# Kernel tuning notes

Measured on AMD Instinct MI355X. Metric: run time of the kernel, lower is better.

Reference implementation:

```python
import jax, jax.numpy as jnp
import numpy as np

H = 256  # GRU hidden size


def _gru_scan(state, lengths, Wih, Whh, bih, bhh):
    # state: [B, T, D]; run a batched GRU over time, freezing h once t >= lengths[b]
    B, T, D = state.shape
    # precompute input gates for all timesteps: [T, B, 3H]
    gi_all = jnp.einsum('btd,gd->tbg', state, Wih) + bih

    def step(h, inp):
        gi, t = inp
        gh = h @ Whh.T + bhh                       # [B, 3H]
        i_r, i_z, i_n = jnp.split(gi, 3, axis=-1)
        h_r, h_z, h_n = jnp.split(gh, 3, axis=-1)
        r = jax.nn.sigmoid(i_r + h_r)
        z = jax.nn.sigmoid(i_z + h_z)
        n = jnp.tanh(i_n + r * h_n)
        h_new = (1.0 - z) * n + z * h              # torch GRUCell update
        mask = (t < lengths)[:, None]              # ragged: stop updating past length
        return jnp.where(mask, h_new, h), None

    h0 = jnp.zeros((B, H), state.dtype)
    h, _ = jax.lax.scan(step, h0, (gi_all, jnp.arange(T)))
    return h  # [B, H] = hidden after lengths[b] GRU steps


def _mlp(x, w1, b1, w2, b2, w3, b3, w4, b4, wq, bq):
    x = jax.nn.relu(x @ w1.T + b1)
    x = jax.nn.relu(x @ w2.T + b2)
    x = jax.nn.relu(x @ w3.T + b3)
    x = jax.nn.relu(x @ w4.T + b4)
    return x @ wq.T + bq  # [B, 1]


def setup_inputs() -> dict:
    key = jax.random.key(0)
    ks = jax.random.split(key, 40)
    B, T, D, A = 2048, 64, 15, 1
    inp = {}
    inp['state'] = jax.random.normal(ks[0], (B, T, D), jnp.float32)
    inp['action'] = jax.random.normal(ks[1], (B, A), jnp.float32)
    inp['lengths'] = jax.random.randint(ks[2], (B,), 1, T + 1, jnp.int32)
    i = 3
    for t in (1, 2):
        for name, shape, fan in [('Wih', (3 * H, D), D), ('Whh', (3 * H, H), H),
                                 ('bih', (3 * H,), H), ('bhh', (3 * H,), H)]:
            inp[f'g{t}_{name}'] = jax.random.normal(ks[i], shape, jnp.float32) / np.sqrt(fan)
            i += 1
        for name, (o, n) in [('fc1', (1024, H + D + A)), ('fc2', (1024, 1024)),
                             ('fc3', (512, 1024)), ('fc4', (256, 512)), ('q', (1, 256))]:
            inp[f'{name}_{t}_w'] = jax.random.normal(ks[i], (o, n), jnp.float32) / np.sqrt(n)
            i += 1
            inp[f'{name}_{t}_b'] = jax.random.normal(ks[i], (o,), jnp.float32) * 0.01
            i += 1
    return inp


def reference(state, action, lengths,
              g1_Wih, g1_Whh, g1_bih, g1_bhh,
              fc1_1_w, fc1_1_b, fc2_1_w, fc2_1_b, fc3_1_w, fc3_1_b,
              fc4_1_w, fc4_1_b, q_1_w, q_1_b,
              g2_Wih, g2_Whh, g2_bih, g2_bhh,
              fc1_2_w, fc1_2_b, fc2_2_w, fc2_2_b, fc3_2_w, fc3_2_b,
              fc4_2_w, fc4_2_b, q_2_w, q_2_b):
    h1 = _gru_scan(state, lengths, g1_Wih, g1_Whh, g1_bih, g1_bhh)
    h2 = _gru_scan(state, lengths, g2_Wih, g2_Whh, g2_bih, g2_bhh)
    aug = jnp.concatenate([state[:, 0, :], action], axis=-1)  # [B, 16]
    x1 = jnp.concatenate([aug, h1], axis=-1)                  # [B, 272]
    x2 = jnp.concatenate([aug, h2], axis=-1)
    out1 = _mlp(x1, fc1_1_w, fc1_1_b, fc2_1_w, fc2_1_b, fc3_1_w, fc3_1_b,
                fc4_1_w, fc4_1_b, q_1_w, q_1_b)
    out2 = _mlp(x2, fc1_2_w, fc1_2_b, fc2_2_w, fc2_2_b, fc3_2_w, fc3_2_b,
                fc4_2_w, fc4_2_b, q_2_w, q_2_b)
    return (out1, out2)
```

## Files before the change

kernel.cpp:

```cpp
#include <hip/hip_runtime.h>

typedef float  f32x4 __attribute__((ext_vector_type(4)));
typedef short  s16x8 __attribute__((ext_vector_type(8)));
typedef __bf16 b16x8 __attribute__((ext_vector_type(8)));
typedef unsigned u32x4 __attribute__((ext_vector_type(4)));

#define DEV __device__ __forceinline__

DEV unsigned short f2b(float f) {
  unsigned u = __builtin_bit_cast(unsigned, f);
  u = (u + 0x7FFFu + ((u >> 16) & 1u)) >> 16;
  return (unsigned short)u;
}
DEV unsigned cvt_pk_bf16(float lo, float hi) {
  unsigned r;
  asm("v_cvt_pk_bf16_f32 %0, %1, %2" : "=v"(r) : "v"(lo), "v"(hi));
  return r;
}
DEV b16x8 ld8(const unsigned short* p) {
  return __builtin_bit_cast(b16x8, *(const s16x8*)p);
}
DEV float sigm(float x) { return __builtin_amdgcn_rcpf(1.f + __expf(-x)); }
DEV float tanh_fast(float x) {
  float e = __expf(2.f * x);
  return 1.f - 2.f * __builtin_amdgcn_rcpf(e + 1.f);
}
DEV void async16(const unsigned short* g, unsigned short* l) {
  __builtin_amdgcn_global_load_lds(
      (const __attribute__((address_space(1))) unsigned int*)g,
      (__attribute__((address_space(3))) unsigned int*)l, 16, 0, 0);
}
DEV f32x4 mfma_bf16(b16x8 a, b16x8 b, f32x4 c) {
  return __builtin_amdgcn_mfma_f32_16x16x32_bf16(a, b, c, 0, 0, 0);
}

struct PrepArgs {
  const float *whh[2], *wih[2], *bih[2], *bhh[2];
  const float *src[2][4];
  unsigned short *waug[2], *dst[2][4];
  const float *qb[2];
  float *out;
};

__global__ __launch_bounds__(256) void prep_kernel(PrepArgs p) {
  const int job = blockIdx.y;
  const int i0 = blockIdx.x * 256 + threadIdx.x;
  const int stride = gridDim.x * 256;
  if (job < 2) {
    const float* whh = p.whh[job];
    const float* wih = p.wih[job];
    const float* bih = p.bih[job];
    const float* bhh = p.bhh[job];
    unsigned short* dst = p.waug[job];
    for (int idx = i0; idx < 768 * 288; idx += stride) {
      int j = idx / 288, k = idx - j * 288;
      float v = 0.f;
      if (k < 256) {
        int o = k & 31;
        int kk = (k & 0x1E0) + (o >> 1) + ((o & 1) << 4);
        v = whh[j * 256 + kk];
      } else if (k < 271)  v = wih[j * 15 + (k - 256)];
      else if (k == 271)   v = (j < 512) ? (bih[j] + bhh[j]) : bih[j];
      dst[idx] = f2b(v);
    }
  } else if (job < 10) {
    const int jj = job - 2, br = jj >> 2, ly = jj & 3;
    const int rowsA[4] = {1024, 1024, 512, 256};
    const int scA[4]   = {272, 1024, 1024, 512};
    const int dcA[4]   = {288, 1024, 1024, 512};
    const float* src = p.src[br][ly];
    unsigned short* dst = p.dst[br][ly];
    const int sc = scA[ly], dc = dcA[ly], tot = rowsA[ly] * dc;
    for (int idx = i0; idx < tot; idx += stride) {
      int r = idx / dc, c = idx - r * dc;
      float v = (c < sc) ? src[r * sc + c] : 0.f;
      dst[idx] = f2b(v);
    }
  } else {
    for (int idx = i0; idx < 4096; idx += stride)
      p.out[idx] = p.qb[idx >> 11][0];
  }
}

#define GRU_LDS_BYTES 147584
__global__ __launch_bounds__(512, 2) void gru_kernel(
    const float* __restrict__ state, const float* __restrict__ action,
    const int* __restrict__ lengths,
    const unsigned short* __restrict__ waug0, const unsigned short* __restrict__ waug1,
    const float* __restrict__ bhh0, const float* __restrict__ bhh1,
    unsigned short* __restrict__ x0, unsigned short* __restrict__ x1) {
  extern __shared__ char smem[];
  unsigned short* W67L = (unsigned short*)smem;
  unsigned short* SgL  = (unsigned short*)(smem + 98304);
  unsigned*       Hb2  = (unsigned*)(smem + 131072);
  int* lenS = (int*)(smem + 147456);
  int* mlS  = (int*)(smem + 147520);
  float* tmpF = (float*)smem;

  const int tid = threadIdx.x;
  const int lane = tid & 63, w = tid >> 6;
  const int l15 = lane & 15, q = lane >> 4;
  const int g = blockIdx.x & 1;
  const int r0 = (blockIdx.x >> 1) * 16;

  const unsigned short* Waug = g ? waug1 : waug0;
  const float* bhh = g ? bhh1 : bhh0;
  unsigned short* xout = g ? x1 : x0;

  {
    const float2* src = (const float2*)(state + (size_t)r0 * 960);
    float2* dstv = (float2*)tmpF;
    for (int i = tid; i < 7680; i += 512) {
      const int row = i / 480;
      dstv[row * 481 + (i - row * 480)] = src[i];
    }
  }
  for (int i = tid; i < 4096; i += 512) Hb2[i] = 0;
  if (tid < 16) lenS[tid] = lengths[r0 + tid];
  __syncthreads();
  if (tid == 0) {
    int m = 1;
    for (int i = 0; i < 16; i++) m = lenS[i] > m ? lenS[i] : m;
    *mlS = m;
  }

  for (int s = tid; s < 64 * 32; s += 512) {
    const int t = s >> 5, L = s & 31;
    const int q2 = L >> 4, r = L & 15;
    const float* bp = tmpF + r * 962 + t * 15;
    unsigned hp[4];
#pragma unroll
    for (int jp = 0; jp < 4; jp++) {
      const int k0 = q2 * 8 + 2 * jp;
      float lo = (k0 < 15) ? bp[k0] : (k0 == 15 ? 1.0f : 0.f);
      float hi = (k0 + 1 < 15) ? bp[k0 + 1] : (k0 + 1 == 15 ? 1.0f : 0.f);
      hp[jp] = cvt_pk_bf16(lo, hi);
    }
    *(u32x4*)(SgL + (size_t)s * 8) = u32x4{hp[0], hp[1], hp[2], hp[3]};
  }
  __syncthreads();

  int c0[6];
  c0[0] = 32 * w;       c0[1] = 32 * w + 16;
  c0[2] = 256 + 32 * w; c0[3] = 256 + 32 * w + 16;
  c0[4] = 512 + 32 * w; c0[5] = 512 + 32 * w + 16;

  b16x8 wres[6][6];
  b16x8 waugf[6];
#pragma unroll
  for (int i = 0; i < 6; i++) {
    const unsigned short* bpi = Waug + (size_t)(c0[i] + l15) * 288 + q * 8;
#pragma unroll
    for (int j = 0; j < 6; j++) wres[i][j] = ld8(bpi + j * 32);
    waugf[i] = ld8(bpi + 256);
#pragma unroll
    for (int ks2 = 0; ks2 < 2; ks2++) {
      b16x8 v = ld8(bpi + (6 + ks2) * 32);
      *(s16x8*)(W67L + (size_t)(ks2 * 6 + i) * 4096 + tid * 8) =
          __builtin_bit_cast(s16x8, v);
    }
  }
  float bnH[2] = {bhh[c0[4] + l15], bhh[c0[5] + l15]};
  int len4[4];
#pragma unroll
  for (int r = 0; r < 4; r++) len4[r] = lenS[q * 4 + r];

  int aOff[8];
#pragma unroll
  for (int j = 0; j < 8; j++) {
    const int cj = 4 * j + q;
    const int pj = (cj & 24) | ((cj & 7) ^ (l15 & 7));
    aOff[j] = l15 * 128 + pj * 4;
  }
  int wOff[4];
#pragma unroll
  for (int rg = 0; rg < 4; rg++) {
    const int row = q * 4 + rg;
    const int cb = 4 * w + (l15 >> 2);
    const int pw = (cb & 24) | ((cb & 7) ^ (row & 7));
    wOff[rg] = row * 128 + pw * 4 + (l15 & 3);
  }
  __syncthreads();
  const int maxlen = *mlS;

  float hold[2][4] = {{0, 0, 0, 0}, {0, 0, 0, 0}};
  int poff = 0;

  for (int t = 0; t < maxlen; ++t) {
    f32x4 acc[6];
    {
      s16x8 raw = *(const s16x8*)(SgL + t * 256 + ((q & 1) * 16 + l15) * 8);
      b16x8 a8 = __builtin_bit_cast(b16x8, raw);
      const f32x4 z4 = {0.f, 0.f, 0.f, 0.f};
#pragma unroll
      for (int i = 0; i < 6; i++) acc[i] = mfma_bf16(a8, waugf[i], z4);
    }
    f32x4 giN0 = acc[4], giN1 = acc[5];
    acc[4] = acc[4] + bnH[0];
    acc[5] = acc[5] + bnH[1];

    __syncthreads();

    const unsigned* hb = Hb2 + poff;
#pragma unroll
    for (int j = 0; j < 6; j++) {
      b16x8 a = __builtin_bit_cast(b16x8, *(const uint4*)(hb + aOff[j]));
#pragma unroll
      for (int i = 0; i < 6; i++) acc[i] = mfma_bf16(a, wres[i][j], acc[i]);
    }
#pragma unroll
    for (int ks2 = 0; ks2 < 2; ks2++) {
      b16x8 a = __builtin_bit_cast(b16x8, *(const uint4*)(hb + aOff[6 + ks2]));
#pragma unroll
      for (int i = 0; i < 6; i++) {
        b16x8 bw = ld8(W67L + (size_t)(ks2 * 6 + i) * 4096 + tid * 8);
        acc[i] = mfma_bf16(a, bw, acc[i]);
      }
    }

    unsigned* hbw = Hb2 + (poff ^ 2048);
#pragma unroll
    for (int rg = 0; rg < 4; rg++) {
      const bool live = (t < len4[rg]);
      float r0g = sigm(acc[0][rg]);
      float z0 = sigm(acc[2][rg]);
      float n0 = tanh_fast(giN0[rg] + r0g * (acc[4][rg] - giN0[rg]));
      float h0 = n0 + z0 * (hold[0][rg] - n0);
      h0 = live ? h0 : hold[0][rg];
      hold[0][rg] = h0;
      float r1g = sigm(acc[1][rg]);
      float z1 = sigm(acc[3][rg]);
      float n1 = tanh_fast(giN1[rg] + r1g * (acc[5][rg] - giN1[rg]));
      float h1 = n1 + z1 * (hold[1][rg] - n1);
      h1 = live ? h1 : hold[1][rg];
      hold[1][rg] = h1;
      hbw[wOff[rg]] = cvt_pk_bf16(h0, h1);
    }
    poff ^= 2048;
  }

#pragma unroll
  for (int i = 0; i < 2; i++) {
    const int c = 32 * w + 16 * i + l15;
#pragma unroll
    for (int rg = 0; rg < 4; rg++) {
      const int row = q * 4 + rg;
      xout[(size_t)(r0 + row) * 288 + 16 + c] = f2b(hold[i][rg]);
    }
  }
  {
    const int row = tid >> 5, cc = tid & 31;
    float v; int col;
    if (cc < 15)       { v = state[(size_t)(r0 + row) * 960 + cc]; col = cc; }
    else if (cc == 15) { v = action[r0 + row]; col = 15; }
    else               { v = 0.f; col = 256 + cc; }
    xout[(size_t)(r0 + row) * 288 + col] = f2b(v);
  }
}

template <int BM, int BN>
__global__ __launch_bounds__(256, 2) void gemm_bias_relu(
    const unsigned short* __restrict__ A0, const unsigned short* __restrict__ A1,
    const unsigned short* __restrict__ W0, const unsigned short* __restrict__ W1,
    const float* __restrict__ b0, const float* __restrict__ b1,
    unsigned short* __restrict__ Y0, unsigned short* __restrict__ Y1,
    int N, int K) {
  const unsigned short* A = blockIdx.z ? A1 : A0;
  const unsigned short* W = blockIdx.z ? W1 : W0;
  const float* bias = blockIdx.z ? b1 : b0;
  unsigned short* Y = blockIdx.z ? Y1 : Y0;

  constexpr int MT = BM / 32;
  constexpr int NT = BN / 32;
  const int tid = threadIdx.x;
  const int lane = tid & 63, wid = tid >> 6;
  const int wm = wid >> 1, wn = wid & 1;
  const int l15 = lane & 15, q = lane >> 4;
  const int m0 = blockIdx.x * BM, n0 = blockIdx.y * BN;

  __shared__ unsigned short As[2][BM * 32];
  __shared__ unsigned short Bs[2][BN * 32];

  f32x4 acc[MT][NT];
#pragma unroll
  for (int mi = 0; mi < MT; mi++)
#pragma unroll
    for (int ni = 0; ni < NT; ni++) acc[mi][ni] = f32x4{0.f, 0.f, 0.f, 0.f};

  const int srow = tid >> 2, scol = (tid & 3) * 8;
  const int nk = K >> 5;

#pragma unroll
  for (int g64 = 0; g64 < BM / 64; g64++)
    async16(A + (size_t)(m0 + g64 * 64 + srow) * K + scol,
            &As[0][g64 * 2048 + tid * 8]);
#pragma unroll
  for (int g64 = 0; g64 < BN / 64; g64++)
    async16(W + (size_t)(n0 + g64 * 64 + srow) * K + scol,
            &Bs[0][g64 * 2048 + tid * 8]);
  __syncthreads();

  for (int t = 0; t < nk; ++t) {
    const int cur = t & 1;
    if (t + 1 < nk) {
      const int k1 = (t + 1) * 32;
#pragma unroll
      for (int g64 = 0; g64 < BM / 64; g64++)
        async16(A + (size_t)(m0 + g64 * 64 + srow) * K + scol + k1,
                &As[cur ^ 1][g64 * 2048 + tid * 8]);
#pragma unroll
      for (int g64 = 0; g64 < BN / 64; g64++)
        async16(W + (size_t)(n0 + g64 * 64 + srow) * K + scol + k1,
                &Bs[cur ^ 1][g64 * 2048 + tid * 8]);
    }

    b16x8 af[MT], bf[NT];
#pragma unroll
    for (int mi = 0; mi < MT; mi++)
      af[mi] = ld8(&As[cur][(wm * (BM / 2) + mi * 16 + l15) * 32 + q * 8]);
#pragma unroll
    for (int ni = 0; ni < NT; ni++)
      bf[ni] = ld8(&Bs[cur][(wn * (BN / 2) + ni * 16 + l15) * 32 + q * 8]);
#pragma unroll
    for (int mi = 0; mi < MT; mi++)
#pragma unroll
      for (int ni = 0; ni < NT; ni++)
        acc[mi][ni] = mfma_bf16(af[mi], bf[ni], acc[mi][ni]);
    __syncthreads();
  }

#pragma unroll
  for (int ni = 0; ni < NT; ni++) {
    const int col = n0 + wn * (BN / 2) + ni * 16 + l15;
    const float bv = bias[col];
#pragma unroll
    for (int mi = 0; mi < MT; mi++) {
      const int rbase = m0 + wm * (BM / 2) + mi * 16 + q * 4;
#pragma unroll
      for (int rg = 0; rg < 4; rg++) {
        float v = acc[mi][ni][rg] + bv;
        v = fmaxf(v, 0.f);
        Y[(size_t)(rbase + rg) * N + col] = f2b(v);
      }
    }
  }
}

__global__ __launch_bounds__(256, 2) void fc4q_kernel(
    const unsigned short* __restrict__ A0, const unsigned short* __restrict__ A1,
    const unsigned short* __restrict__ W0, const unsigned short* __restrict__ W1,
    const float* __restrict__ b0, const float* __restrict__ b1,
    const float* __restrict__ qw0, const float* __restrict__ qw1,
    float* __restrict__ out) {
  const unsigned short* A = blockIdx.z ? A1 : A0;
  const unsigned short* W = blockIdx.z ? W1 : W0;
  const float* bias = blockIdx.z ? b1 : b0;
  const float* qw = blockIdx.z ? qw1 : qw0;

  const int tid = threadIdx.x;
  const int lane = tid & 63, wn = tid >> 6;
  const int l15 = lane & 15, q = lane >> 4;
  const int m0 = blockIdx.x * 32;
  const int nbase = blockIdx.y * 128;
  const int K = 512;

  __shared__ unsigned short As[2][32 * 32];
  __shared__ unsigned short Bs[2][128 * 32];
  __shared__ float red[32][4];

  f32x4 acc[2][2];
#pragma unroll
  for (int mi = 0; mi < 2; mi++)
#pragma unroll
    for (int ni = 0; ni < 2; ni++) acc[mi][ni] = f32x4{0.f, 0.f, 0.f, 0.f};

  const int srow = tid >> 2, scol = (tid & 3) * 8;
  const int nk = K >> 5;

  if (tid < 128)
    async16(A + (size_t)(m0 + srow) * K + scol, &As[0][tid * 8]);
#pragma unroll
  for (int g64 = 0; g64 < 2; g64++)
    async16(W + (size_t)(nbase + g64 * 64 + srow) * K + scol,
            &Bs[0][g64 * 2048 + tid * 8]);
  __syncthreads();

  for (int t = 0; t < nk; ++t) {
    const int cur = t & 1;
    if (t + 1 < nk) {
      const int k1 = (t + 1) * 32;
      if (tid < 128)
        async16(A + (size_t)(m0 + srow) * K + scol + k1, &As[cur ^ 1][tid * 8]);
#pragma unroll
      for (int g64 = 0; g64 < 2; g64++)
        async16(W + (size_t)(nbase + g64 * 64 + srow) * K + scol + k1,
                &Bs[cur ^ 1][g64 * 2048 + tid * 8]);
    }

    b16x8 af[2], bf[2];
#pragma unroll
    for (int mi = 0; mi < 2; mi++)
      af[mi] = ld8(&As[cur][(mi * 16 + l15) * 32 + q * 8]);
#pragma unroll
    for (int ni = 0; ni < 2; ni++)
      bf[ni] = ld8(&Bs[cur][(wn * 32 + ni * 16 + l15) * 32 + q * 8]);
#pragma unroll
    for (int mi = 0; mi < 2; mi++)
#pragma unroll
      for (int ni = 0; ni < 2; ni++)
        acc[mi][ni] = mfma_bf16(af[mi], bf[ni], acc[mi][ni]);
    __syncthreads();
  }

#pragma unroll
  for (int mi = 0; mi < 2; mi++) {
#pragma unroll
    for (int rg = 0; rg < 4; rg++) {
      float s = 0.f;
#pragma unroll
      for (int ni = 0; ni < 2; ni++) {
        const int col = nbase + wn * 32 + ni * 16 + l15;
        float v = fmaxf(acc[mi][ni][rg] + bias[col], 0.f);
        s += v * qw[col];
      }
#pragma unroll
      for (int off = 1; off < 16; off <<= 1) s += __shfl_xor(s, off);
      if (l15 == 0) red[mi * 16 + q * 4 + rg][wn] = s;
    }
  }
  __syncthreads();
  if (tid < 32) {
    float t = red[tid][0] + red[tid][1] + red[tid][2] + red[tid][3];
    atomicAdd(out + (size_t)blockIdx.z * 2048 + m0 + tid, t);
  }
}

extern "C" void kernel_launch(void* const* d_in, const int* in_sizes, int n_in,
                              void* d_out, int out_size, void* d_ws, size_t ws_size,
                              hipStream_t stream) {
  const float* state   = (const float*)d_in[0];
  const float* action  = (const float*)d_in[1];
  const int*   lengths = (const int*)d_in[2];
  const float* g_wih[2] = {(const float*)d_in[3], (const float*)d_in[17]};
  const float* g_whh[2] = {(const float*)d_in[4], (const float*)d_in[18]};
  const float* g_bih[2] = {(const float*)d_in[5], (const float*)d_in[19]};
  const float* g_bhh[2] = {(const float*)d_in[6], (const float*)d_in[20]};
  const float* fcw[2][4] = {
      {(const float*)d_in[7], (const float*)d_in[9], (const float*)d_in[11], (const float*)d_in[13]},
      {(const float*)d_in[21], (const float*)d_in[23], (const float*)d_in[25], (const float*)d_in[27]}};
  const float* fcb[2][4] = {
      {(const float*)d_in[8], (const float*)d_in[10], (const float*)d_in[12], (const float*)d_in[14]},
      {(const float*)d_in[22], (const float*)d_in[24], (const float*)d_in[26], (const float*)d_in[28]}};
  const float* qw[2] = {(const float*)d_in[15], (const float*)d_in[29]};
  const float* qb[2] = {(const float*)d_in[16], (const float*)d_in[30]};
  float* out = (float*)d_out;

  uintptr_t base = (uintptr_t)d_ws;
  auto alloc = [&](size_t bytes) -> unsigned short* {
    void* p = (void*)base;
    base += (bytes + 255) & ~(size_t)255;
    return (unsigned short*)p;
  };
  unsigned short *waug[2], *w1b[2], *w2b[2], *w3b[2], *w4b[2], *xb[2], *yA[2], *yB[2];
  for (int g = 0; g < 2; g++) waug[g] = alloc(768 * 288 * 2);
  for (int g = 0; g < 2; g++) w1b[g] = alloc(1024 * 288 * 2);
  for (int g = 0; g < 2; g++) w2b[g] = alloc(1024 * 1024 * 2);
  for (int g = 0; g < 2; g++) w3b[g] = alloc(512 * 1024 * 2);
  for (int g = 0; g < 2; g++) w4b[g] = alloc(256 * 512 * 2);
  for (int g = 0; g < 2; g++) xb[g] = alloc(2048 * 288 * 2);
  for (int g = 0; g < 2; g++) yA[g] = alloc(2048 * 1024 * 2);
  for (int g = 0; g < 2; g++) yB[g] = alloc(2048 * 1024 * 2);
  (void)ws_size; (void)in_sizes; (void)n_in; (void)out_size;

  PrepArgs pa;
  for (int g = 0; g < 2; g++) {
    pa.whh[g] = g_whh[g]; pa.wih[g] = g_wih[g];
    pa.bih[g] = g_bih[g]; pa.bhh[g] = g_bhh[g];
    pa.waug[g] = waug[g];
    pa.src[g][0] = fcw[g][0]; pa.dst[g][0] = w1b[g];
    pa.src[g][1] = fcw[g][1]; pa.dst[g][1] = w2b[g];
    pa.src[g][2] = fcw[g][2]; pa.dst[g][2] = w3b[g];
    pa.src[g][3] = fcw[g][3]; pa.dst[g][3] = w4b[g];
    pa.qb[g] = qb[g];
  }
  pa.out = out;
  prep_kernel<<<dim3(64, 11), 256, 0, stream>>>(pa);

  (void)hipFuncSetAttribute((const void*)gru_kernel,
                            hipFuncAttributeMaxDynamicSharedMemorySize,
                            GRU_LDS_BYTES);
  gru_kernel<<<dim3(256), dim3(512), GRU_LDS_BYTES, stream>>>(
      state, action, lengths, waug[0], waug[1], g_bhh[0], g_bhh[1], xb[0], xb[1]);

  gemm_bias_relu<64, 128><<<dim3(32, 8, 2), 256, 0, stream>>>(
      xb[0], xb[1], w1b[0], w1b[1], fcb[0][0], fcb[1][0], yA[0], yA[1], 1024, 288);
  gemm_bias_relu<64, 128><<<dim3(32, 8, 2), 256, 0, stream>>>(
      yA[0], yA[1], w2b[0], w2b[1], fcb[0][1], fcb[1][1], yB[0], yB[1], 1024, 1024);
  gemm_bias_relu<64, 64><<<dim3(32, 8, 2), 256, 0, stream>>>(
      yB[0], yB[1], w3b[0], w3b[1], fcb[0][2], fcb[1][2], yA[0], yA[1], 512, 1024);
  fc4q_kernel<<<dim3(64, 2, 2), 256, 0, stream>>>(
      yA[0], yA[1], w4b[0], w4b[1], fcb[0][3], fcb[1][3], qw[0], qw[1], out);
}
```

Measured before the change: 310.6 us.

## Fuse four MLP layers and Q head into one LDS-resident kernel

Replaces the three tiled GEMM launches and the fc4+q kernel with a single mlp_kernel. Each 512-thread block owns 32 rows of one branch and keeps the intermediate activations in swizzled LDS, so the 2048x1024 bf16 intermediates never go through global memory. Weights for layers 2-4 are permuted during prep so the k-interleaved activation layout matches, and the output bias init plus atomics become direct stores. The risk is that only 128 blocks run, each streaming every weight matrix straight from global/L2 without LDS staging, which lowers parallelism and adds repeated weight traffic.

```diff
diff --git a/kernel.cpp b/kernel.cpp
--- a/kernel.cpp
+++ b/kernel.cpp
@@ -25,11 +25,6 @@
   float e = __expf(2.f * x);
   return 1.f - 2.f * __builtin_amdgcn_rcpf(e + 1.f);
 }
-DEV void async16(const unsigned short* g, unsigned short* l) {
-  __builtin_amdgcn_global_load_lds(
-      (const __attribute__((address_space(1))) unsigned int*)g,
-      (__attribute__((address_space(3))) unsigned int*)l, 16, 0, 0);
-}
 DEV f32x4 mfma_bf16(b16x8 a, b16x8 b, f32x4 c) {
   return __builtin_amdgcn_mfma_f32_16x16x32_bf16(a, b, c, 0, 0, 0);
 }
@@ -38,8 +33,6 @@
   const float *whh[2], *wih[2], *bih[2], *bhh[2];
   const float *src[2][4];
   unsigned short *waug[2], *dst[2][4];
-  const float *qb[2];
-  float *out;
 };
 
 __global__ __launch_bounds__(256) void prep_kernel(PrepArgs p) {
@@ -63,7 +56,7 @@
       else if (k == 271)   v = (j < 512) ? (bih[j] + bhh[j]) : bih[j];
       dst[idx] = f2b(v);
     }
-  } else if (job < 10) {
+  } else {
     const int jj = job - 2, br = jj >> 2, ly = jj & 3;
     const int rowsA[4] = {1024, 1024, 512, 256};
     const int scA[4]   = {272, 1024, 1024, 512};
@@ -73,12 +66,16 @@
     const int sc = scA[ly], dc = dcA[ly], tot = rowsA[ly] * dc;
     for (int idx = i0; idx < tot; idx += stride) {
       int r = idx / dc, c = idx - r * dc;
-      float v = (c < sc) ? src[r * sc + c] : 0.f;
+      float v;
+      if (ly == 0) {
+        v = (c < sc) ? src[r * sc + c] : 0.f;
+      } else {
+        int o = c & 31;
+        int kk = (c & ~31) + (o >> 1) + ((o & 1) << 4);
+        v = src[r * sc + kk];
+      }
       dst[idx] = f2b(v);
     }
-  } else {
-    for (int idx = i0; idx < 4096; idx += stride)
-      p.out[idx] = p.qb[idx >> 11][0];
   }
 }
 
@@ -258,180 +255,162 @@
   }
 }
 
-template <int BM, int BN>
-__global__ __launch_bounds__(256, 2) void gemm_bias_relu(
-    const unsigned short* __restrict__ A0, const unsigned short* __restrict__ A1,
-    const unsigned short* __restrict__ W0, const unsigned short* __restrict__ W1,
-    const float* __restrict__ b0, const float* __restrict__ b1,
-    unsigned short* __restrict__ Y0, unsigned short* __restrict__ Y1,
-    int N, int K) {
-  const unsigned short* A = blockIdx.z ? A1 : A0;
-  const unsigned short* W = blockIdx.z ? W1 : W0;
-  const float* bias = blockIdx.z ? b1 : b0;
-  unsigned short* Y = blockIdx.z ? Y1 : Y0;
-
-  constexpr int MT = BM / 32;
-  constexpr int NT = BN / 32;
+struct MlpArgs {
+  const unsigned short *x[2], *w1[2], *w2[2], *w3[2], *w4[2];
+  const float *b1[2], *b2[2], *b3[2], *b4[2], *qw[2], *qb[2];
+  float* out;
+};
+
+#define MLP_LDS_BYTES 131584
+__global__ __launch_bounds__(512, 2) void mlp_kernel(MlpArgs p) {
+  extern __shared__ char smem[];
+  unsigned* Y1 = (unsigned*)smem;
+  unsigned* Y2 = (unsigned*)(smem + 65536);
+  float* red = (float*)(smem + 131072);
+
   const int tid = threadIdx.x;
-  const int lane = tid & 63, wid = tid >> 6;
-  const int wm = wid >> 1, wn = wid & 1;
+  const int lane = tid & 63, w = tid >> 6;
   const int l15 = lane & 15, q = lane >> 4;
-  const int m0 = blockIdx.x * BM, n0 = blockIdx.y * BN;
-
-  __shared__ unsigned short As[2][BM * 32];
-  __shared__ unsigned short Bs[2][BN * 32];
-
-  f32x4 acc[MT][NT];
-#pragma unroll
-  for (int mi = 0; mi < MT; mi++)
-#pragma unroll
-    for (int ni = 0; ni < NT; ni++) acc[mi][ni] = f32x4{0.f, 0.f, 0.f, 0.f};
-
-  const int srow = tid >> 2, scol = (tid & 3) * 8;
-  const int nk = K >> 5;
-
-#pragma unroll
-  for (int g64 = 0; g64 < BM / 64; g64++)
-    async16(A + (size_t)(m0 + g64 * 64 + srow) * K + scol,
-            &As[0][g64 * 2048 + tid * 8]);
-#pragma unroll
-  for (int g64 = 0; g64 < BN / 64; g64++)
-    async16(W + (size_t)(n0 + g64 * 64 + srow) * K + scol,
-            &Bs[0][g64 * 2048 + tid * 8]);
-  __syncthreads();
-
-  for (int t = 0; t < nk; ++t) {
-    const int cur = t & 1;
-    if (t + 1 < nk) {
-      const int k1 = (t + 1) * 32;
-#pragma unroll
-      for (int g64 = 0; g64 < BM / 64; g64++)
-        async16(A + (size_t)(m0 + g64 * 64 + srow) * K + scol + k1,
-                &As[cur ^ 1][g64 * 2048 + tid * 8]);
-#pragma unroll
-      for (int g64 = 0; g64 < BN / 64; g64++)
-        async16(W + (size_t)(n0 + g64 * 64 + srow) * K + scol + k1,
-                &Bs[cur ^ 1][g64 * 2048 + tid * 8]);
-    }
-
-    b16x8 af[MT], bf[NT];
-#pragma unroll
-    for (int mi = 0; mi < MT; mi++)
-      af[mi] = ld8(&As[cur][(wm * (BM / 2) + mi * 16 + l15) * 32 + q * 8]);
-#pragma unroll
-    for (int ni = 0; ni < NT; ni++)
-      bf[ni] = ld8(&Bs[cur][(wn * (BN / 2) + ni * 16 + l15) * 32 + q * 8]);
-#pragma unroll
-    for (int mi = 0; mi < MT; mi++)
-#pragma unroll
-      for (int ni = 0; ni < NT; ni++)
-        acc[mi][ni] = mfma_bf16(af[mi], bf[ni], acc[mi][ni]);
-    __syncthreads();
-  }
-
-#pragma unroll
-  for (int ni = 0; ni < NT; ni++) {
-    const int col = n0 + wn * (BN / 2) + ni * 16 + l15;
-    const float bv = bias[col];
-#pragma unroll
-    for (int mi = 0; mi < MT; mi++) {
-      const int rbase = m0 + wm * (BM / 2) + mi * 16 + q * 4;
+  const int h = w >> 2, cq = w & 3;
+  const int g = blockIdx.x & 1;
+  const int r0 = (blockIdx.x >> 1) * 32;
+  const int Rr = h * 16 + l15;
+
+  f32x4 acc[16];
+
+#pragma unroll
+  for (int nt = 0; nt < 16; nt++) acc[nt] = f32x4{0.f, 0.f, 0.f, 0.f};
+  {
+    b16x8 af[9];
+    const unsigned short* xp =
+        p.x[g] + (size_t)(r0 + h * 16 + l15) * 288 + q * 8;
+#pragma unroll
+    for (int j = 0; j < 9; j++) af[j] = ld8(xp + j * 32);
+    const unsigned short* w1p = p.w1[g] + (size_t)(cq * 256 + l15) * 288 + q * 8;
+#pragma unroll
+    for (int j = 0; j < 9; j++)
+#pragma unroll
+      for (int nt = 0; nt < 16; nt++)
+        acc[nt] = mfma_bf16(af[j], ld8(w1p + (size_t)nt * 16 * 288 + j * 32),
+                            acc[nt]);
+    const float* b1 = p.b1[g];
+#pragma unroll
+    for (int ntp = 0; ntp < 8; ntp++) {
+      const int colL = cq * 256 + ntp * 32 + l15;
+      const float bv0 = b1[colL], bv1 = b1[colL + 16];
+      const int cb = (cq * 8 + ntp) * 4 + (l15 >> 2);
 #pragma unroll
       for (int rg = 0; rg < 4; rg++) {
-        float v = acc[mi][ni][rg] + bv;
-        v = fmaxf(v, 0.f);
-        Y[(size_t)(rbase + rg) * N + col] = f2b(v);
-      }
-    }
-  }
-}
-
-__global__ __launch_bounds__(256, 2) void fc4q_kernel(
-    const unsigned short* __restrict__ A0, const unsigned short* __restrict__ A1,
-    const unsigned short* __restrict__ W0, const unsigned short* __restrict__ W1,
-    const float* __restrict__ b0, const float* __restrict__ b1,
-    const float* __restrict__ qw0, const float* __restrict__ qw1,
-    float* __restrict__ out) {
-  const unsigned short* A = blockIdx.z ? A1 : A0;
-  const unsigned short* W = blockIdx.z ? W1 : W0;
-  const float* bias = blockIdx.z ? b1 : b0;
-  const float* qw = blockIdx.z ? qw1 : qw0;
-
-  const int tid = threadIdx.x;
-  const int lane = tid & 63, wn = tid >> 6;
-  const int l15 = lane & 15, q = lane >> 4;
-  const int m0 = blockIdx.x * 32;
-  const int nbase = blockIdx.y * 128;
-  const int K = 512;
-
-  __shared__ unsigned short As[2][32 * 32];
-  __shared__ unsigned short Bs[2][128 * 32];
-  __shared__ float red[32][4];
-
-  f32x4 acc[2][2];
-#pragma unroll
-  for (int mi = 0; mi < 2; mi++)
-#pragma unroll
-    for (int ni = 0; ni < 2; ni++) acc[mi][ni] = f32x4{0.f, 0.f, 0.f, 0.f};
-
-  const int srow = tid >> 2, scol = (tid & 3) * 8;
-  const int nk = K >> 5;
-
-  if (tid < 128)
-    async16(A + (size_t)(m0 + srow) * K + scol, &As[0][tid * 8]);
-#pragma unroll
-  for (int g64 = 0; g64 < 2; g64++)
-    async16(W + (size_t)(nbase + g64 * 64 + srow) * K + scol,
-            &Bs[0][g64 * 2048 + tid * 8]);
-  __syncthreads();
-
-  for (int t = 0; t < nk; ++t) {
-    const int cur = t & 1;
-    if (t + 1 < nk) {
-      const int k1 = (t + 1) * 32;
-      if (tid < 128)
-        async16(A + (size_t)(m0 + srow) * K + scol + k1, &As[cur ^ 1][tid * 8]);
-#pragma unroll
-      for (int g64 = 0; g64 < 2; g64++)
-        async16(W + (size_t)(nbase + g64 * 64 + srow) * K + scol + k1,
-                &Bs[cur ^ 1][g64 * 2048 + tid * 8]);
-    }
-
-    b16x8 af[2], bf[2];
-#pragma unroll
-    for (int mi = 0; mi < 2; mi++)
-      af[mi] = ld8(&As[cur][(mi * 16 + l15) * 32 + q * 8]);
-#pragma unroll
-    for (int ni = 0; ni < 2; ni++)
-      bf[ni] = ld8(&Bs[cur][(wn * 32 + ni * 16 + l15) * 32 + q * 8]);
-#pragma unroll
-    for (int mi = 0; mi < 2; mi++)
-#pragma unroll
-      for (int ni = 0; ni < 2; ni++)
-        acc[mi][ni] = mfma_bf16(af[mi], bf[ni], acc[mi][ni]);
-    __syncthreads();
-  }
-
-#pragma unroll
-  for (int mi = 0; mi < 2; mi++) {
+        const int R = h * 16 + q * 4 + rg;
+        float v0 = fmaxf(acc[2 * ntp][rg] + bv0, 0.f);
+        float v1 = fmaxf(acc[2 * ntp + 1][rg] + bv1, 0.f);
+        const int pw = (cb & 120) | ((cb & 7) ^ (R & 7));
+        Y1[R * 512 + pw * 4 + (l15 & 3)] = cvt_pk_bf16(v0, v1);
+      }
+    }
+  }
+  __syncthreads();
+
+#pragma unroll
+  for (int nt = 0; nt < 16; nt++) acc[nt] = f32x4{0.f, 0.f, 0.f, 0.f};
+  {
+    const unsigned* y1r = Y1 + Rr * 512;
+    const unsigned short* w2p = p.w2[g] + (size_t)(cq * 256 + l15) * 1024 + q * 8;
+    for (int j2 = 0; j2 < 32; ++j2) {
+      const int cj = j2 * 4 + q;
+      const int pj = (cj & 120) | ((cj & 7) ^ (l15 & 7));
+      b16x8 a = __builtin_bit_cast(b16x8, *(const uint4*)(y1r + pj * 4));
+#pragma unroll
+      for (int nt = 0; nt < 16; nt++)
+        acc[nt] = mfma_bf16(a, ld8(w2p + (size_t)nt * 16 * 1024 + j2 * 32),
+                            acc[nt]);
+    }
+    const float* b2 = p.b2[g];
+#pragma unroll
+    for (int ntp = 0; ntp < 8; ntp++) {
+      const int colL = cq * 256 + ntp * 32 + l15;
+      const float bv0 = b2[colL], bv1 = b2[colL + 16];
+      const int cb = (cq * 8 + ntp) * 4 + (l15 >> 2);
+#pragma unroll
+      for (int rg = 0; rg < 4; rg++) {
+        const int R = h * 16 + q * 4 + rg;
+        float v0 = fmaxf(acc[2 * ntp][rg] + bv0, 0.f);
+        float v1 = fmaxf(acc[2 * ntp + 1][rg] + bv1, 0.f);
+        const int pw = (cb & 120) | ((cb & 7) ^ (R & 7));
+        Y2[R * 512 + pw * 4 + (l15 & 3)] = cvt_pk_bf16(v0, v1);
+      }
+    }
+  }
+  __syncthreads();
+
+  unsigned* Y3 = Y1;
+#pragma unroll
+  for (int nt = 0; nt < 8; nt++) acc[nt] = f32x4{0.f, 0.f, 0.f, 0.f};
+  {
+    const unsigned* y2r = Y2 + Rr * 512;
+    const unsigned short* w3p = p.w3[g] + (size_t)(cq * 128 + l15) * 1024 + q * 8;
+    for (int j2 = 0; j2 < 32; ++j2) {
+      const int cj = j2 * 4 + q;
+      const int pj = (cj & 120) | ((cj & 7) ^ (l15 & 7));
+      b16x8 a = __builtin_bit_cast(b16x8, *(const uint4*)(y2r + pj * 4));
+#pragma unroll
+      for (int nt = 0; nt < 8; nt++)
+        acc[nt] = mfma_bf16(a, ld8(w3p + (size_t)nt * 16 * 1024 + j2 * 32),
+                            acc[nt]);
+    }
+    const float* b3 = p.b3[g];
+#pragma unroll
+    for (int ntp = 0; ntp < 4; ntp++) {
+      const int colL = cq * 128 + ntp * 32 + l15;
+      const float bv0 = b3[colL], bv1 = b3[colL + 16];
+      const int cb = (cq * 4 + ntp) * 4 + (l15 >> 2);
+#pragma unroll
+      for (int rg = 0; rg < 4; rg++) {
+        const int R = h * 16 + q * 4 + rg;
+        float v0 = fmaxf(acc[2 * ntp][rg] + bv0, 0.f);
+        float v1 = fmaxf(acc[2 * ntp + 1][rg] + bv1, 0.f);
+        const int pw = (cb & 56) | ((cb & 7) ^ (R & 7));
+        Y3[R * 256 + pw * 4 + (l15 & 3)] = cvt_pk_bf16(v0, v1);
+      }
+    }
+  }
+  __syncthreads();
+
+#pragma unroll
+  for (int nt = 0; nt < 4; nt++) acc[nt] = f32x4{0.f, 0.f, 0.f, 0.f};
+  {
+    const unsigned* y3r = Y3 + Rr * 256;
+    const unsigned short* w4p = p.w4[g] + (size_t)(cq * 64 + l15) * 512 + q * 8;
+    for (int j4 = 0; j4 < 16; ++j4) {
+      const int cj = j4 * 4 + q;
+      const int pj = (cj & 56) | ((cj & 7) ^ (l15 & 7));
+      b16x8 a = __builtin_bit_cast(b16x8, *(const uint4*)(y3r + pj * 4));
+#pragma unroll
+      for (int nt = 0; nt < 4; nt++)
+        acc[nt] = mfma_bf16(a, ld8(w4p + (size_t)nt * 16 * 512 + j4 * 32),
+                            acc[nt]);
+    }
+    const float* b4 = p.b4[g];
+    const float* qw = p.qw[g];
 #pragma unroll
     for (int rg = 0; rg < 4; rg++) {
       float s = 0.f;
 #pragma unroll
-      for (int ni = 0; ni < 2; ni++) {
-        const int col = nbase + wn * 32 + ni * 16 + l15;
-        float v = fmaxf(acc[mi][ni][rg] + bias[col], 0.f);
+      for (int nt = 0; nt < 4; nt++) {
+        const int col = cq * 64 + nt * 16 + l15;
+        float v = fmaxf(acc[nt][rg] + b4[col], 0.f);
         s += v * qw[col];
       }
 #pragma unroll
       for (int off = 1; off < 16; off <<= 1) s += __shfl_xor(s, off);
-      if (l15 == 0) red[mi * 16 + q * 4 + rg][wn] = s;
+      if (l15 == 0) red[(h * 16 + q * 4 + rg) * 4 + cq] = s;
     }
   }
   __syncthreads();
   if (tid < 32) {
-    float t = red[tid][0] + red[tid][1] + red[tid][2] + red[tid][3];
-    atomicAdd(out + (size_t)blockIdx.z * 2048 + m0 + tid, t);
+    float t = red[tid * 4] + red[tid * 4 + 1] + red[tid * 4 + 2] +
+              red[tid * 4 + 3] + p.qb[g][0];
+    p.out[(size_t)g * 2048 + r0 + tid] = t;
   }
 }
 
@@ -461,15 +440,13 @@
     base += (bytes + 255) & ~(size_t)255;
     return (unsigned short*)p;
   };
-  unsigned short *waug[2], *w1b[2], *w2b[2], *w3b[2], *w4b[2], *xb[2], *yA[2], *yB[2];
+  unsigned short *waug[2], *w1b[2], *w2b[2], *w3b[2], *w4b[2], *xb[2];
   for (int g = 0; g < 2; g++) waug[g] = alloc(768 * 288 * 2);
   for (int g = 0; g < 2; g++) w1b[g] = alloc(1024 * 288 * 2);
   for (int g = 0; g < 2; g++) w2b[g] = alloc(1024 * 1024 * 2);
   for (int g = 0; g < 2; g++) w3b[g] = alloc(512 * 1024 * 2);
   for (int g = 0; g < 2; g++) w4b[g] = alloc(256 * 512 * 2);
   for (int g = 0; g < 2; g++) xb[g] = alloc(2048 * 288 * 2);
-  for (int g = 0; g < 2; g++) yA[g] = alloc(2048 * 1024 * 2);
-  for (int g = 0; g < 2; g++) yB[g] = alloc(2048 * 1024 * 2);
   (void)ws_size; (void)in_sizes; (void)n_in; (void)out_size;
 
   PrepArgs pa;
@@ -481,10 +458,8 @@
     pa.src[g][1] = fcw[g][1]; pa.dst[g][1] = w2b[g];
     pa.src[g][2] = fcw[g][2]; pa.dst[g][2] = w3b[g];
     pa.src[g][3] = fcw[g][3]; pa.dst[g][3] = w4b[g];
-    pa.qb[g] = qb[g];
-  }
-  pa.out = out;
-  prep_kernel<<<dim3(64, 11), 256, 0, stream>>>(pa);
+  }
+  prep_kernel<<<dim3(64, 10), 256, 0, stream>>>(pa);
 
   (void)hipFuncSetAttribute((const void*)gru_kernel,
                             hipFuncAttributeMaxDynamicSharedMemorySize,
@@ -492,12 +467,17 @@
   gru_kernel<<<dim3(256), dim3(512), GRU_LDS_BYTES, stream>>>(
       state, action, lengths, waug[0], waug[1], g_bhh[0], g_bhh[1], xb[0], xb[1]);
 
-  gemm_bias_relu<64, 128><<<dim3(32, 8, 2), 256, 0, stream>>>(
-      xb[0], xb[1], w1b[0], w1b[1], fcb[0][0], fcb[1][0], yA[0], yA[1], 1024, 288);
-  gemm_bias_relu<64, 128><<<dim3(32, 8, 2), 256, 0, stream>>>(
-      yA[0], yA[1], w2b[0], w2b[1], fcb[0][1], fcb[1][1], yB[0], yB[1], 1024, 1024);
-  gemm_bias_relu<64, 64><<<dim3(32, 8, 2), 256, 0, stream>>>(
-      yB[0], yB[1], w3b[0], w3b[1], fcb[0][2], fcb[1][2], yA[0], yA[1], 512, 1024);
-  fc4q_kernel<<<dim3(64, 2, 2), 256, 0, stream>>>(
-      yA[0], yA[1], w4b[0], w4b[1], fcb[0][3], fcb[1][3], qw[0], qw[1], out);
-}
+  MlpArgs ma;
+  for (int g = 0; g < 2; g++) {
+    ma.x[g] = xb[g];
+    ma.w1[g] = w1b[g]; ma.w2[g] = w2b[g]; ma.w3[g] = w3b[g]; ma.w4[g] = w4b[g];
+    ma.b1[g] = fcb[g][0]; ma.b2[g] = fcb[g][1];
+    ma.b3[g] = fcb[g][2]; ma.b4[g] = fcb[g][3];
+    ma.qw[g] = qw[g]; ma.qb[g] = qb[g];
+  }
+  ma.out = out;
+  (void)hipFuncSetAttribute((const void*)mlp_kernel,
+                            hipFuncAttributeMaxDynamicSharedMemorySize,
+                            MLP_LDS_BYTES);
+  mlp_kernel<<<dim3(128), dim3(512), MLP_LDS_BYTES, stream>>>(ma);
+}
```

Result: slower. 468.9 us (+51.0%).

## Halve GRU block to 256 threads, each wave owning twice the hidden columns

Applied to the files above, without the earlier changes.

The GRU recurrence kernel now runs with 4 waves instead of 8 per block. Each wave handles 64 hidden columns (12 gate tiles) instead of 32, so register-resident weights double to 72 bf16x8 fragments per lane, and the per-step work is split into two halves with separate gate updates. The aim is to make the per-timestep barrier cheaper with fewer waves and to reuse each h fragment load across more MFMAs. The cost is heavy register pressure that risks spills, and less latency hiding within the serial time loop.

```diff
diff --git a/kernel.cpp b/kernel.cpp
--- a/kernel.cpp
+++ b/kernel.cpp
@@ -83,7 +83,7 @@
 }
 
 #define GRU_LDS_BYTES 147584
-__global__ __launch_bounds__(512, 2) void gru_kernel(
+__global__ __launch_bounds__(256, 1) void gru_kernel(
     const float* __restrict__ state, const float* __restrict__ action,
     const int* __restrict__ lengths,
     const unsigned short* __restrict__ waug0, const unsigned short* __restrict__ waug1,
@@ -110,12 +110,12 @@
   {
     const float2* src = (const float2*)(state + (size_t)r0 * 960);
     float2* dstv = (float2*)tmpF;
-    for (int i = tid; i < 7680; i += 512) {
+    for (int i = tid; i < 7680; i += 256) {
       const int row = i / 480;
       dstv[row * 481 + (i - row * 480)] = src[i];
     }
   }
-  for (int i = tid; i < 4096; i += 512) Hb2[i] = 0;
+  for (int i = tid; i < 4096; i += 256) Hb2[i] = 0;
   if (tid < 16) lenS[tid] = lengths[r0 + tid];
   __syncthreads();
   if (tid == 0) {
@@ -124,7 +124,7 @@
     *mlS = m;
   }
 
-  for (int s = tid; s < 64 * 32; s += 512) {
+  for (int s = tid; s < 64 * 32; s += 256) {
     const int t = s >> 5, L = s & 31;
     const int q2 = L >> 4, r = L & 15;
     const float* bp = tmpF + r * 962 + t * 15;
@@ -140,15 +140,14 @@
   }
   __syncthreads();
 
-  int c0[6];
-  c0[0] = 32 * w;       c0[1] = 32 * w + 16;
-  c0[2] = 256 + 32 * w; c0[3] = 256 + 32 * w + 16;
-  c0[4] = 512 + 32 * w; c0[5] = 512 + 32 * w + 16;
-
-  b16x8 wres[6][6];
-  b16x8 waugf[6];
-#pragma unroll
-  for (int i = 0; i < 6; i++) {
+  int c0[12];
+#pragma unroll
+  for (int i = 0; i < 12; i++) c0[i] = (i >> 2) * 256 + 64 * w + 16 * (i & 3);
+
+  b16x8 wres[12][6];
+  b16x8 waugf[12];
+#pragma unroll
+  for (int i = 0; i < 12; i++) {
     const unsigned short* bpi = Waug + (size_t)(c0[i] + l15) * 288 + q * 8;
 #pragma unroll
     for (int j = 0; j < 6; j++) wres[i][j] = ld8(bpi + j * 32);
@@ -156,11 +155,13 @@
 #pragma unroll
     for (int ks2 = 0; ks2 < 2; ks2++) {
       b16x8 v = ld8(bpi + (6 + ks2) * 32);
-      *(s16x8*)(W67L + (size_t)(ks2 * 6 + i) * 4096 + tid * 8) =
+      *(s16x8*)(W67L + (size_t)(ks2 * 12 + i) * 2048 + tid * 8) =
           __builtin_bit_cast(s16x8, v);
     }
   }
-  float bnH[2] = {bhh[c0[4] + l15], bhh[c0[5] + l15]};
+  float bnH[4];
+#pragma unroll
+  for (int p = 0; p < 4; p++) bnH[p] = bhh[c0[8 + p] + l15];
   int len4[4];
 #pragma unroll
   for (int r = 0; r < 4; r++) len4[r] = lenS[q * 4 + r];
@@ -172,84 +173,101 @@
     const int pj = (cj & 24) | ((cj & 7) ^ (l15 & 7));
     aOff[j] = l15 * 128 + pj * 4;
   }
-  int wOff[4];
-#pragma unroll
-  for (int rg = 0; rg < 4; rg++) {
-    const int row = q * 4 + rg;
-    const int cb = 4 * w + (l15 >> 2);
-    const int pw = (cb & 24) | ((cb & 7) ^ (row & 7));
-    wOff[rg] = row * 128 + pw * 4 + (l15 & 3);
+  int wOff[2][4];
+#pragma unroll
+  for (int pp = 0; pp < 2; pp++) {
+    const int cb = 4 * (2 * w + pp) + (l15 >> 2);
+#pragma unroll
+    for (int rg = 0; rg < 4; rg++) {
+      const int row = q * 4 + rg;
+      const int pw = (cb & 24) | ((cb & 7) ^ (row & 7));
+      wOff[pp][rg] = row * 128 + pw * 4 + (l15 & 3);
+    }
   }
   __syncthreads();
   const int maxlen = *mlS;
 
-  float hold[2][4] = {{0, 0, 0, 0}, {0, 0, 0, 0}};
+  float hold[4][4] = {{0,0,0,0},{0,0,0,0},{0,0,0,0},{0,0,0,0}};
   int poff = 0;
 
   for (int t = 0; t < maxlen; ++t) {
-    f32x4 acc[6];
+    f32x4 acc[12];
     {
       s16x8 raw = *(const s16x8*)(SgL + t * 256 + ((q & 1) * 16 + l15) * 8);
       b16x8 a8 = __builtin_bit_cast(b16x8, raw);
       const f32x4 z4 = {0.f, 0.f, 0.f, 0.f};
 #pragma unroll
-      for (int i = 0; i < 6; i++) acc[i] = mfma_bf16(a8, waugf[i], z4);
-    }
-    f32x4 giN0 = acc[4], giN1 = acc[5];
-    acc[4] = acc[4] + bnH[0];
-    acc[5] = acc[5] + bnH[1];
+      for (int i = 0; i < 12; i++) acc[i] = mfma_bf16(a8, waugf[i], z4);
+    }
+    f32x4 giN[4];
+#pragma unroll
+    for (int p = 0; p < 4; p++) {
+      giN[p] = acc[8 + p];
+      acc[8 + p] = acc[8 + p] + bnH[p];
+    }
 
     __syncthreads();
 
     const unsigned* hb = Hb2 + poff;
-#pragma unroll
-    for (int j = 0; j < 6; j++) {
-      b16x8 a = __builtin_bit_cast(b16x8, *(const uint4*)(hb + aOff[j]));
-#pragma unroll
-      for (int i = 0; i < 6; i++) acc[i] = mfma_bf16(a, wres[i][j], acc[i]);
-    }
-#pragma unroll
-    for (int ks2 = 0; ks2 < 2; ks2++) {
-      b16x8 a = __builtin_bit_cast(b16x8, *(const uint4*)(hb + aOff[6 + ks2]));
-#pragma unroll
-      for (int i = 0; i < 6; i++) {
-        b16x8 bw = ld8(W67L + (size_t)(ks2 * 6 + i) * 4096 + tid * 8);
-        acc[i] = mfma_bf16(a, bw, acc[i]);
+    unsigned* hbw = Hb2 + (poff ^ 2048);
+
+#pragma unroll
+    for (int pp = 0; pp < 2; ++pp) {
+      const int p0 = 2 * pp, p1 = 2 * pp + 1;
+#pragma unroll
+      for (int j = 0; j < 8; ++j) {
+        b16x8 a = __builtin_bit_cast(b16x8, *(const uint4*)(hb + aOff[j]));
+        if (j < 6) {
+          acc[p0]     = mfma_bf16(a, wres[p0][j],     acc[p0]);
+          acc[p1]     = mfma_bf16(a, wres[p1][j],     acc[p1]);
+          acc[4 + p0] = mfma_bf16(a, wres[4 + p0][j], acc[4 + p0]);
+          acc[4 + p1] = mfma_bf16(a, wres[4 + p1][j], acc[4 + p1]);
+          acc[8 + p0] = mfma_bf16(a, wres[8 + p0][j], acc[8 + p0]);
+          acc[8 + p1] = mfma_bf16(a, wres[8 + p1][j], acc[8 + p1]);
+        } else {
+          const int ks2 = j - 6;
+          const unsigned short* ab = W67L + (size_t)ks2 * 12 * 2048 + tid * 8;
+          acc[p0]     = mfma_bf16(a, ld8(ab + (size_t)(p0)     * 2048), acc[p0]);
+          acc[p1]     = mfma_bf16(a, ld8(ab + (size_t)(p1)     * 2048), acc[p1]);
+          acc[4 + p0] = mfma_bf16(a, ld8(ab + (size_t)(4 + p0) * 2048), acc[4 + p0]);
+          acc[4 + p1] = mfma_bf16(a, ld8(ab + (size_t)(4 + p1) * 2048), acc[4 + p1]);
+          acc[8 + p0] = mfma_bf16(a, ld8(ab + (size_t)(8 + p0) * 2048), acc[8 + p0]);
+          acc[8 + p1] = mfma_bf16(a, ld8(ab + (size_t)(8 + p1) * 2048), acc[8 + p1]);
+        }
       }
-    }
-
-    unsigned* hbw = Hb2 + (poff ^ 2048);
-#pragma unroll
-    for (int rg = 0; rg < 4; rg++) {
-      const bool live = (t < len4[rg]);
-      float r0g = sigm(acc[0][rg]);
-      float z0 = sigm(acc[2][rg]);
-      float n0 = tanh_fast(giN0[rg] + r0g * (acc[4][rg] - giN0[rg]));
-      float h0 = n0 + z0 * (hold[0][rg] - n0);
-      h0 = live ? h0 : hold[0][rg];
-      hold[0][rg] = h0;
-      float r1g = sigm(acc[1][rg]);
-      float z1 = sigm(acc[3][rg]);
-      float n1 = tanh_fast(giN1[rg] + r1g * (acc[5][rg] - giN1[rg]));
-      float h1 = n1 + z1 * (hold[1][rg] - n1);
-      h1 = live ? h1 : hold[1][rg];
-      hold[1][rg] = h1;
-      hbw[wOff[rg]] = cvt_pk_bf16(h0, h1);
+#pragma unroll
+      for (int rg = 0; rg < 4; ++rg) {
+        const bool live = (t < len4[rg]);
+        float rA = sigm(acc[p0][rg]);
+        float zA = sigm(acc[4 + p0][rg]);
+        float nA = tanh_fast(giN[p0][rg] + rA * (acc[8 + p0][rg] - giN[p0][rg]));
+        float hA = nA + zA * (hold[p0][rg] - nA);
+        hA = live ? hA : hold[p0][rg];
+        hold[p0][rg] = hA;
+        float rB = sigm(acc[p1][rg]);
+        float zB = sigm(acc[4 + p1][rg]);
+        float nB = tanh_fast(giN[p1][rg] + rB * (acc[8 + p1][rg] - giN[p1][rg]));
+        float hB = nB + zB * (hold[p1][rg] - nB);
+        hB = live ? hB : hold[p1][rg];
+        hold[p1][rg] = hB;
+        hbw[wOff[pp][rg]] = cvt_pk_bf16(hA, hB);
+      }
     }
     poff ^= 2048;
   }
 
 #pragma unroll
-  for (int i = 0; i < 2; i++) {
-    const int c = 32 * w + 16 * i + l15;
+  for (int p = 0; p < 4; p++) {
+    const int c = 64 * w + 16 * p + l15;
 #pragma unroll
     for (int rg = 0; rg < 4; rg++) {
       const int row = q * 4 + rg;
-      xout[(size_t)(r0 + row) * 288 + 16 + c] = f2b(hold[i][rg]);
-    }
-  }
-  {
-    const int row = tid >> 5, cc = tid & 31;
+      xout[(size_t)(r0 + row) * 288 + 16 + c] = f2b(hold[p][rg]);
+    }
+  }
+#pragma unroll
+  for (int half = 0; half < 2; half++) {
+    const int row = (tid >> 5) + half * 8, cc = tid & 31;
     float v; int col;
     if (cc < 15)       { v = state[(size_t)(r0 + row) * 960 + cc]; col = cc; }
     else if (cc == 15) { v = action[r0 + row]; col = 15; }
@@ -489,7 +507,7 @@
   (void)hipFuncSetAttribute((const void*)gru_kernel,
                             hipFuncAttributeMaxDynamicSharedMemorySize,
                             GRU_LDS_BYTES);
-  gru_kernel<<<dim3(256), dim3(512), GRU_LDS_BYTES, stream>>>(
+  gru_kernel<<<dim3(256), dim3(256), GRU_LDS_BYTES, stream>>>(
       state, action, lengths, waug[0], waug[1], g_bhh[0], g_bhh[1], xb[0], xb[1]);
 
   gemm_bias_relu<64, 128><<<dim3(32, 8, 2), 256, 0, stream>>>(
```

Result: slower. 392.8 us (+26.5%).
